# Optimization experiments

Hardware: AMD Instinct MI355X
Metric: run time of the kernel (lower is better)

Reference implementation:

```python
import jax, jax.numpy as jnp
import numpy as np

COMMITMENT_COST = 0.25
NUM_EMBEDDINGS = 1024
EMBEDDING_DIM = 64


def setup_inputs() -> dict:
    key = jax.random.key(0)
    k1, k2 = jax.random.split(key)
    x = jax.random.normal(k1, (32, 64, 64, 64), dtype=jnp.float32)
    embeddings = jax.random.normal(k2, (EMBEDDING_DIM, NUM_EMBEDDINGS), dtype=jnp.float32)
    return {"x": x, "embeddings": embeddings}


def reference(x, embeddings):
    # x: [..., D], embeddings: [D, K]
    flat = jnp.reshape(x, (-1, EMBEDDING_DIM))                       # [N, D]
    # squared euclidean distances via ||a||^2 - 2 a.e + ||e||^2      # [N, K]
    distances = (jnp.sum(flat * flat, axis=1, keepdims=True)
                 - 2.0 * (flat @ embeddings)
                 + jnp.sum(embeddings * embeddings, axis=0, keepdims=True))
    flat_indices = jnp.argmax(-distances, axis=1)                    # [N]
    encodings = jax.nn.one_hot(flat_indices, NUM_EMBEDDINGS, dtype=distances.dtype)  # [N, K]
    encoding_indices = jnp.reshape(flat_indices, x.shape[:-1])
    # gather codebook rows: embeddings.T[idx]
    quantized = jnp.take(embeddings.T, encoding_indices, axis=0)     # same shape as x
    e_latent_loss = jnp.mean((jax.lax.stop_gradient(quantized) - x) ** 2)
    q_latent_loss = jnp.mean((quantized - jax.lax.stop_gradient(x)) ** 2)
    loss = q_latent_loss + COMMITMENT_COST * e_latent_loss
    quantized_st = x + jax.lax.stop_gradient(quantized - x)          # straight-through
    avg_probs = jnp.mean(encodings, axis=0)                          # [K]
    perplexity = jnp.exp(-jnp.sum(avg_probs * jnp.log(avg_probs + 1e-10)))
    return quantized_st, loss, perplexity, encodings, encoding_indices, distances
```

## Files before the change

### kernel.cpp

```cpp
#include <hip/hip_runtime.h>
#include <hip/hip_bf16.h>
#include <math.h>

#define NROWS 131072
#define DDIM  64
#define KCODE 1024
#define TAU_B 0.008f

#define OFF_Q    0L
#define OFF_LOSS 8388608L
#define OFF_PERP 8388609L
#define OFF_ENC  8388610L
#define OFF_IDX  (OFF_ENC + 134217728L)
#define OFF_DIST (OFF_IDX + 131072L)

#define WS_ENORM 0L
#define WS_ET    1024L
#define WS_EBPH  66560L
#define WS_EBPL  99328L
#define WS_IDX   132096L
#define WS_CNT   263168L
#define WS_PART  395268L

typedef short bf16x8 __attribute__((ext_vector_type(8)));
typedef float f32x4  __attribute__((ext_vector_type(4)));
typedef float f32x2  __attribute__((ext_vector_type(2)));
typedef _Float16 f16x4v __attribute__((ext_vector_type(4)));

__device__ inline unsigned short f2bf(float f) {
    unsigned u = __float_as_uint(f);
    unsigned r = (u + 0x7fffu + ((u >> 16) & 1u)) >> 16;
    return (unsigned short)r;
}
__device__ inline float bf2f(unsigned short h) {
    return __uint_as_float(((unsigned)h) << 16);
}
__device__ inline int dswz16(int i) { return i ^ (((i >> 12) & 3) << 3); }

__global__ __launch_bounds__(256) void k1a_prep(const float* __restrict__ e,
                                                float* __restrict__ enorm,
                                                float* __restrict__ eT,
                                                int* __restrict__ cnt) {
    int k = blockIdx.x * 256 + threadIdx.x;
    float s = 0.f;
    #pragma unroll 8
    for (int d = 0; d < DDIM; ++d) {
        float v = e[(size_t)d * KCODE + k];
        s = fmaf(v, v, s);
        eT[(size_t)k * DDIM + d] = v;
    }
    enorm[k] = s;
    cnt[k] = 0;
}

__global__ __launch_bounds__(128) void k1b_pack(const float* __restrict__ e,
                                                unsigned short* __restrict__ ebph,
                                                unsigned short* __restrict__ ebpl) {
    const int gct = blockIdx.x;
    const int ks  = threadIdx.x >> 6;
    const int l   = threadIdx.x & 63;
    const int col = (gct << 4) | (l & 15);
    const int kb  = (ks << 5) + ((l >> 4) << 3);
    const size_t ob = ((size_t)((gct << 1) | ks) * 64 + l) * 8;
    #pragma unroll
    for (int j = 0; j < 8; ++j) {
        float f = e[(size_t)(kb + j) * KCODE + col];
        unsigned short h = f2bf(f);
        float lo = f - bf2f(h);
        ebph[ob + j] = h;
        ebpl[ob + j] = f2bf(lo);
    }
}

__global__ __launch_bounds__(256, 4) void kA_dist(const float* __restrict__ x,
                                                  const float* __restrict__ e,
                                                  const unsigned short* __restrict__ ebph,
                                                  const unsigned short* __restrict__ ebpl,
                                                  const float* __restrict__ enorm,
                                                  float* __restrict__ dist,
                                                  int* __restrict__ idxarr,
                                                  int* __restrict__ cnt,
                                                  float* __restrict__ partials) {
    __shared__ __align__(16) _Float16 dtH[16384];
    __shared__ float hd[2];
    __shared__ short xh[16 * 64];
    __shared__ short xl[16 * 64];
    __shared__ float xn[16];
    __shared__ float wm1[4][16], wm2[4][16];
    __shared__ int   wi1[4][16];
    __shared__ float ps[16];
    __shared__ int   sidx[16];
    __shared__ int   nearmask;
    __shared__ float xsh[DDIM];
    __shared__ double wbv[4];
    __shared__ int    wbi[4];

    const int tid  = threadIdx.x;
    const int lane = tid & 63;
    const int w    = tid >> 6;
    const int rowbase = blockIdx.x * 16;

    {
        if (tid == 0) nearmask = 0;
        float4 v = ((const float4*)(x + (size_t)rowbase * DDIM))[tid];
        int fi = tid * 4, r = fi >> 6, c = fi & 63;
        float fv[4] = {v.x, v.y, v.z, v.w};
        short hv[4], lv[4];
        #pragma unroll
        for (int q = 0; q < 4; ++q) {
            unsigned short hh = f2bf(fv[q]);
            hv[q] = (short)hh;
            lv[q] = (short)f2bf(fv[q] - bf2f(hh));
        }
        *(short4*)&xh[r * 64 + c] = make_short4(hv[0], hv[1], hv[2], hv[3]);
        *(short4*)&xl[r * 64 + c] = make_short4(lv[0], lv[1], lv[2], lv[3]);
        float s4 = fmaf(v.x, v.x, fmaf(v.y, v.y, fmaf(v.z, v.z, v.w * v.w)));
        #pragma unroll
        for (int m = 1; m < 16; m <<= 1) s4 += __shfl_xor(s4, m);
        if ((lane & 15) == 0) xn[r] = s4;
    }
    __syncthreads();

    const int arow = lane & 15, akb = (lane >> 4) << 3;
    bf16x8 ah0 = *(const bf16x8*)&xh[arow * 64 + akb];
    bf16x8 ah1 = *(const bf16x8*)&xh[arow * 64 + 32 + akb];
    bf16x8 al0 = *(const bf16x8*)&xl[arow * 64 + akb];
    bf16x8 al1 = *(const bf16x8*)&xl[arow * 64 + 32 + akb];

    const int wr   = (lane >> 4) << 2;
    const int colb = (w << 8) | (lane & 15);
    float xnv[4];
    #pragma unroll
    for (int r = 0; r < 4; ++r) xnv[r] = xn[wr + r];
    float env[16];
    #pragma unroll
    for (int ct = 0; ct < 16; ++ct) env[ct] = enorm[colb + (ct << 4)];

    float m1[4], m2[4];
    int   i1[4];
    #pragma unroll
    for (int r = 0; r < 4; ++r) { m1[r] = 3.4e38f; m2[r] = 3.4e38f; i1[r] = 1 << 30; }

    #pragma unroll 4
    for (int ct = 0; ct < 16; ++ct) {
        const int gct = (w << 4) | ct;
        const size_t bo = ((size_t)(gct << 1) * 64 + lane) * 8;
        bf16x8 bh0 = *(const bf16x8*)(ebph + bo);
        bf16x8 bh1 = *(const bf16x8*)(ebph + bo + 512);
        bf16x8 bl0 = *(const bf16x8*)(ebpl + bo);
        bf16x8 bl1 = *(const bf16x8*)(ebpl + bo + 512);

        f32x4 d = {0.f, 0.f, 0.f, 0.f};
        d = __builtin_amdgcn_mfma_f32_16x16x32_bf16(ah0, bh0, d, 0, 0, 0);
        d = __builtin_amdgcn_mfma_f32_16x16x32_bf16(ah1, bh1, d, 0, 0, 0);
        d = __builtin_amdgcn_mfma_f32_16x16x32_bf16(ah0, bl0, d, 0, 0, 0);
        d = __builtin_amdgcn_mfma_f32_16x16x32_bf16(ah1, bl1, d, 0, 0, 0);
        d = __builtin_amdgcn_mfma_f32_16x16x32_bf16(al0, bh0, d, 0, 0, 0);
        d = __builtin_amdgcn_mfma_f32_16x16x32_bf16(al1, bh1, d, 0, 0, 0);

        const int col = colb + (ct << 4);
        #pragma unroll
        for (int r = 0; r < 4; ++r) {
            float o = fmaf(-2.f, d[r], xnv[r] + env[ct]);
            if (o < m1[r]) { m2[r] = m1[r]; m1[r] = o; i1[r] = col; }
            else if (o < m2[r]) m2[r] = o;
            const int fl = ((wr + r) << 10) + col;
            if (fl >= 2) dtH[dswz16(fl - 2)] = (_Float16)o;
            else         hd[fl] = o;
        }
    }

    #pragma unroll
    for (int m = 1; m < 16; m <<= 1) {
        #pragma unroll
        for (int r = 0; r < 4; ++r) {
            float om1 = __shfl_xor(m1[r], m);
            int   oi1 = __shfl_xor(i1[r], m);
            float om2 = __shfl_xor(m2[r], m);
            if (om1 < m1[r] || (om1 == m1[r] && oi1 < i1[r])) {
                m2[r] = fminf(m1[r], om2); m1[r] = om1; i1[r] = oi1;
            } else {
                m2[r] = fminf(m2[r], om1);
            }
        }
    }
    if ((lane & 15) == 0) {
        #pragma unroll
        for (int r = 0; r < 4; ++r) {
            wm1[w][wr + r] = m1[r];
            wm2[w][wr + r] = m2[r];
            wi1[w][wr + r] = i1[r];
        }
    }
    __syncthreads();
    if (tid < 16) {
        float bm1 = wm1[0][tid], bm2 = wm2[0][tid];
        int   bi  = wi1[0][tid];
        #pragma unroll
        for (int wv = 1; wv < 4; ++wv) {
            float om1 = wm1[wv][tid], om2 = wm2[wv][tid];
            int   oi  = wi1[wv][tid];
            if (om1 < bm1 || (om1 == bm1 && oi < bi)) {
                bm2 = fminf(bm1, om2); bm1 = om1; bi = oi;
            } else {
                bm2 = fminf(bm2, om1);
            }
        }
        sidx[tid] = bi;
        ps[tid]   = bm1;
        if (bm2 - bm1 < TAU_B) atomicOr(&nearmask, 1 << tid);
    }
    __syncthreads();

    {
        float* dbase = dist + ((size_t)rowbase << 10);
        #pragma unroll
        for (int j = 0; j < 16; ++j) {
            const int s = (j << 8) + tid;
            if (s < 4095) {
                const int i0 = s << 2;
                const int iw = dswz16(i0);
                f16x4v h = *(const f16x4v*)&dtH[iw];
                f32x4 v = {(float)h[0], (float)h[1], (float)h[2], (float)h[3]};
                *(f32x4*)(dbase + 2 + i0) = v;
            }
        }
        if (tid == 255) {
            const int it = dswz16(16380);
            *(f32x2*)(dbase)         = (f32x2){hd[0], hd[1]};
            *(f32x2*)(dbase + 16382) = (f32x2){(float)dtH[it], (float)dtH[it + 1]};
        }
    }

    if (nearmask) {
        for (int mrow = nearmask; mrow; mrow &= (mrow - 1)) {
            const int r = __ffs(mrow) - 1;
            if (tid < DDIM) xsh[tid] = x[(size_t)(rowbase + r) * DDIM + tid];
            __syncthreads();
            const int k0 = tid * 4;
            double dd[4] = {0.0, 0.0, 0.0, 0.0};
            for (int d = 0; d < DDIM; ++d) {
                double xd = (double)xsh[d];
                float4 ev = *(const float4*)(e + (size_t)d * KCODE + k0);
                double t0 = xd - (double)ev.x; dd[0] = fma(t0, t0, dd[0]);
                double t1 = xd - (double)ev.y; dd[1] = fma(t1, t1, dd[1]);
                double t2 = xd - (double)ev.z; dd[2] = fma(t2, t2, dd[2]);
                double t3 = xd - (double)ev.w; dd[3] = fma(t3, t3, dd[3]);
            }
            double best = dd[0]; int bidx = k0;
            #pragma unroll
            for (int c = 1; c < 4; ++c)
                if (dd[c] < best) { best = dd[c]; bidx = k0 + c; }
            #pragma unroll
            for (int m = 1; m < 64; m <<= 1) {
                double ob = __shfl_xor(best, m);
                int    oi = __shfl_xor(bidx, m);
                if (ob < best || (ob == best && oi < bidx)) { best = ob; bidx = oi; }
            }
            if (lane == 0) { wbv[w] = best; wbi[w] = bidx; }
            __syncthreads();
            if (tid == 0) {
                double bb = wbv[0]; int bi = wbi[0];
                #pragma unroll
                for (int wv = 1; wv < 4; ++wv)
                    if (wbv[wv] < bb || (wbv[wv] == bb && wbi[wv] < bi)) {
                        bb = wbv[wv]; bi = wbi[wv];
                    }
                sidx[r] = bi; ps[r] = (float)bb;
            }
            __syncthreads();
        }
    }

    if (tid < 16) {
        const int idx = sidx[tid];
        idxarr[rowbase + tid] = idx;
        atomicAdd(cnt + idx, 1);
    }
    if (tid == 64) {
        float s = 0.f;
        #pragma unroll
        for (int j = 0; j < 16; ++j) s += ps[j];
        partials[blockIdx.x] = s;
    }
}

__global__ __launch_bounds__(256) void kC_final(const float* __restrict__ eT,
                                                const int* __restrict__ idxarr,
                                                float* __restrict__ outq,
                                                float* __restrict__ enc,
                                                float* __restrict__ outidx) {
    __shared__ int sidx[64];
    const int tid = threadIdx.x;
    const int rowbase = blockIdx.x * 64;

    if (tid < 64) {
        const int grow = rowbase + tid;
        const int idx = idxarr[grow];
        sidx[tid] = idx;
        outidx[grow] = (float)idx;
    }
    __syncthreads();

    #pragma unroll
    for (int it = 0; it < 4; ++it) {
        const int row = (it << 4) + (tid >> 4);
        const int grow = rowbase + row;
        const int idx = sidx[row];
        f32x4 ev = *(const f32x4*)(eT + (size_t)idx * DDIM + ((tid & 15) << 2));
        *((f32x4*)(outq + ((size_t)grow << 6)) + (tid & 15)) = ev;
    }

    float* ebase = enc + ((size_t)rowbase << 10);
    #pragma unroll 8
    for (int j = 0; j < 64; ++j) {
        const int s = (j << 8) + tid;
        if (s < 16383) {
            const int fb = 2 + (s << 2);
            const int r0 = fb >> 10, c0 = fb & 1023;
            const int i0 = sidx[r0];
            f32x4 v;
            if (c0 != 1022) {
                v.x = (c0     == i0) ? 1.f : 0.f;
                v.y = (c0 + 1 == i0) ? 1.f : 0.f;
                v.z = (c0 + 2 == i0) ? 1.f : 0.f;
                v.w = (c0 + 3 == i0) ? 1.f : 0.f;
            } else {
                const int i1b = sidx[r0 + 1];
                v.x = (1022 == i0)  ? 1.f : 0.f;
                v.y = (1023 == i0)  ? 1.f : 0.f;
                v.z = (0    == i1b) ? 1.f : 0.f;
                v.w = (1    == i1b) ? 1.f : 0.f;
            }
            *(f32x4*)(ebase + fb) = v;
        }
    }
    if (tid == 255) {
        f32x2 h, t;
        h.x = (0 == sidx[0]) ? 1.f : 0.f;
        h.y = (1 == sidx[0]) ? 1.f : 0.f;
        t.x = (1022 == sidx[63]) ? 1.f : 0.f;
        t.y = (1023 == sidx[63]) ? 1.f : 0.f;
        *(f32x2*)(ebase) = h;
        *(f32x2*)(ebase + 65534) = t;
    }
}

__global__ __launch_bounds__(256) void k6_scalar(const float* __restrict__ partials,
                                                 const int* __restrict__ cnt,
                                                 float* __restrict__ outloss,
                                                 float* __restrict__ outperp) {
    __shared__ double sd[256];
    const int tid = threadIdx.x;
    double s = 0.0;
    for (int i = tid; i < 8192; i += 256) s += (double)partials[i];
    sd[tid] = s;
    __syncthreads();
    for (int st = 128; st > 0; st >>= 1) {
        if (tid < st) sd[tid] += sd[tid + st];
        __syncthreads();
    }
    const double total = sd[0];
    __syncthreads();
    double h = 0.0;
    for (int k = tid; k < KCODE; k += 256) {
        double p = (double)cnt[k] / (double)NROWS;
        h -= p * log(p + 1e-10);
    }
    sd[tid] = h;
    __syncthreads();
    for (int st = 128; st > 0; st >>= 1) {
        if (tid < st) sd[tid] += sd[tid + st];
        __syncthreads();
    }
    if (tid == 0) {
        *outloss = (float)(total * 1.25 / (double)((long)NROWS * DDIM));
        *outperp = (float)exp(sd[0]);
    }
}

extern "C" void kernel_launch(void* const* d_in, const int* in_sizes, int n_in,
                              void* d_out, int out_size, void* d_ws, size_t ws_size,
                              hipStream_t stream) {
    const float* x = (const float*)d_in[0];
    const float* e = (const float*)d_in[1];
    float* out = (float*)d_out;

    float* ws_f = (float*)d_ws;
    float* enorm   = ws_f + WS_ENORM;
    float* eT      = ws_f + WS_ET;
    unsigned short* ebph = (unsigned short*)(ws_f + WS_EBPH);
    unsigned short* ebpl = (unsigned short*)(ws_f + WS_EBPL);
    int*   idxarr  = (int*)(ws_f + WS_IDX);
    int*   cnt     = (int*)(ws_f + WS_CNT);
    float* partials= ws_f + WS_PART;

    float* outq    = out + OFF_Q;
    float* outloss = out + OFF_LOSS;
    float* outperp = out + OFF_PERP;
    float* enc     = out + OFF_ENC;
    float* outidx  = out + OFF_IDX;
    float* dist    = out + OFF_DIST;

    hipLaunchKernelGGL(k1a_prep, dim3(4),    dim3(256), 0, stream, e, enorm, eT, cnt);
    hipLaunchKernelGGL(k1b_pack, dim3(64),   dim3(128), 0, stream, e, ebph, ebpl);
    hipLaunchKernelGGL(kA_dist,  dim3(8192), dim3(256), 0, stream, x, e, ebph, ebpl, enorm,
                       dist, idxarr, cnt, partials);
    hipLaunchKernelGGL(kC_final, dim3(2048), dim3(256), 0, stream, eT, idxarr, outq, enc, outidx);
    hipLaunchKernelGGL(k6_scalar,dim3(1),    dim3(256), 0, stream, partials, cnt, outloss, outperp);
}
```

Before: 339.9 us.

## Swap MFMA operands and write distances directly from registers, dropping LDS staging

Swaps the MFMA A/B operands so each lane holds four consecutive codebook columns for a single row. The fp32 distances can then go straight from registers to global memory as 8-byte stores, with no fp16 LDS staging buffer and no separate copy-out pass. Codebook norms are cached in LDS and read as float4, and the per-row min reduction becomes a cross-lane shuffle over the row groups. The aim is to cut LDS traffic, the fp16 truncation of stored distances and a block-wide pass, but the direct stores are narrower and strided across rows, which may lower write coalescing.

```diff
diff --git a/kernel.cpp b/kernel.cpp
--- a/kernel.cpp
+++ b/kernel.cpp
@@ -25,7 +25,6 @@
 typedef short bf16x8 __attribute__((ext_vector_type(8)));
 typedef float f32x4  __attribute__((ext_vector_type(4)));
 typedef float f32x2  __attribute__((ext_vector_type(2)));
-typedef _Float16 f16x4v __attribute__((ext_vector_type(4)));
 
 __device__ inline unsigned short f2bf(float f) {
     unsigned u = __float_as_uint(f);
@@ -35,7 +34,6 @@
 __device__ inline float bf2f(unsigned short h) {
     return __uint_as_float(((unsigned)h) << 16);
 }
-__device__ inline int dswz16(int i) { return i ^ (((i >> 12) & 3) << 3); }
 
 __global__ __launch_bounds__(256) void k1a_prep(const float* __restrict__ e,
                                                 float* __restrict__ enorm,
@@ -81,10 +79,9 @@
                                                   int* __restrict__ idxarr,
                                                   int* __restrict__ cnt,
                                                   float* __restrict__ partials) {
-    __shared__ __align__(16) _Float16 dtH[16384];
-    __shared__ float hd[2];
     __shared__ short xh[16 * 64];
     __shared__ short xl[16 * 64];
+    __shared__ float enl[KCODE];
     __shared__ float xn[16];
     __shared__ float wm1[4][16], wm2[4][16];
     __shared__ int   wi1[4][16];
@@ -118,6 +115,7 @@
         #pragma unroll
         for (int m = 1; m < 16; m <<= 1) s4 += __shfl_xor(s4, m);
         if ((lane & 15) == 0) xn[r] = s4;
+        ((float4*)enl)[tid] = ((const float4*)enorm)[tid];
     }
     __syncthreads();
 
@@ -127,19 +125,13 @@
     bf16x8 al0 = *(const bf16x8*)&xl[arow * 64 + akb];
     bf16x8 al1 = *(const bf16x8*)&xl[arow * 64 + 32 + akb];
 
-    const int wr   = (lane >> 4) << 2;
-    const int colb = (w << 8) | (lane & 15);
-    float xnv[4];
-    #pragma unroll
-    for (int r = 0; r < 4; ++r) xnv[r] = xn[wr + r];
-    float env[16];
-    #pragma unroll
-    for (int ct = 0; ct < 16; ++ct) env[ct] = enorm[colb + (ct << 4)];
-
-    float m1[4], m2[4];
-    int   i1[4];
-    #pragma unroll
-    for (int r = 0; r < 4; ++r) { m1[r] = 3.4e38f; m2[r] = 3.4e38f; i1[r] = 1 << 30; }
+    const int xr = lane & 15;
+    const int wr = (lane >> 4) << 2;
+    const float xnv = xn[xr];
+    float* drow = dist + (size_t)(rowbase + xr) * KCODE + (w << 8) + wr;
+
+    float m1 = 3.4e38f, m2 = 3.4e38f;
+    int   i1 = 1 << 30;
 
     #pragma unroll 4
     for (int ct = 0; ct < 16; ++ct) {
@@ -151,47 +143,41 @@
         bf16x8 bl1 = *(const bf16x8*)(ebpl + bo + 512);
 
         f32x4 d = {0.f, 0.f, 0.f, 0.f};
-        d = __builtin_amdgcn_mfma_f32_16x16x32_bf16(ah0, bh0, d, 0, 0, 0);
-        d = __builtin_amdgcn_mfma_f32_16x16x32_bf16(ah1, bh1, d, 0, 0, 0);
-        d = __builtin_amdgcn_mfma_f32_16x16x32_bf16(ah0, bl0, d, 0, 0, 0);
-        d = __builtin_amdgcn_mfma_f32_16x16x32_bf16(ah1, bl1, d, 0, 0, 0);
-        d = __builtin_amdgcn_mfma_f32_16x16x32_bf16(al0, bh0, d, 0, 0, 0);
-        d = __builtin_amdgcn_mfma_f32_16x16x32_bf16(al1, bh1, d, 0, 0, 0);
-
-        const int col = colb + (ct << 4);
-        #pragma unroll
-        for (int r = 0; r < 4; ++r) {
-            float o = fmaf(-2.f, d[r], xnv[r] + env[ct]);
-            if (o < m1[r]) { m2[r] = m1[r]; m1[r] = o; i1[r] = col; }
-            else if (o < m2[r]) m2[r] = o;
-            const int fl = ((wr + r) << 10) + col;
-            if (fl >= 2) dtH[dswz16(fl - 2)] = (_Float16)o;
-            else         hd[fl] = o;
-        }
+        d = __builtin_amdgcn_mfma_f32_16x16x32_bf16(bh0, ah0, d, 0, 0, 0);
+        d = __builtin_amdgcn_mfma_f32_16x16x32_bf16(bh1, ah1, d, 0, 0, 0);
+        d = __builtin_amdgcn_mfma_f32_16x16x32_bf16(bl0, ah0, d, 0, 0, 0);
+        d = __builtin_amdgcn_mfma_f32_16x16x32_bf16(bl1, ah1, d, 0, 0, 0);
+        d = __builtin_amdgcn_mfma_f32_16x16x32_bf16(bh0, al0, d, 0, 0, 0);
+        d = __builtin_amdgcn_mfma_f32_16x16x32_bf16(bh1, al1, d, 0, 0, 0);
+
+        const int cb = (w << 8) + (ct << 4) + wr;
+        f32x4 en4 = *(const f32x4*)&enl[cb];
+        float o0 = fmaf(-2.f, d[0], xnv + en4[0]);
+        float o1 = fmaf(-2.f, d[1], xnv + en4[1]);
+        float o2 = fmaf(-2.f, d[2], xnv + en4[2]);
+        float o3 = fmaf(-2.f, d[3], xnv + en4[3]);
+
+        *(f32x2*)(drow + (ct << 4))     = (f32x2){o0, o1};
+        *(f32x2*)(drow + (ct << 4) + 2) = (f32x2){o2, o3};
+
+        if (o0 < m1) { m2 = m1; m1 = o0; i1 = cb; }     else if (o0 < m2) m2 = o0;
+        if (o1 < m1) { m2 = m1; m1 = o1; i1 = cb + 1; } else if (o1 < m2) m2 = o1;
+        if (o2 < m1) { m2 = m1; m1 = o2; i1 = cb + 2; } else if (o2 < m2) m2 = o2;
+        if (o3 < m1) { m2 = m1; m1 = o3; i1 = cb + 3; } else if (o3 < m2) m2 = o3;
     }
 
     #pragma unroll
-    for (int m = 1; m < 16; m <<= 1) {
-        #pragma unroll
-        for (int r = 0; r < 4; ++r) {
-            float om1 = __shfl_xor(m1[r], m);
-            int   oi1 = __shfl_xor(i1[r], m);
-            float om2 = __shfl_xor(m2[r], m);
-            if (om1 < m1[r] || (om1 == m1[r] && oi1 < i1[r])) {
-                m2[r] = fminf(m1[r], om2); m1[r] = om1; i1[r] = oi1;
-            } else {
-                m2[r] = fminf(m2[r], om1);
-            }
-        }
-    }
-    if ((lane & 15) == 0) {
-        #pragma unroll
-        for (int r = 0; r < 4; ++r) {
-            wm1[w][wr + r] = m1[r];
-            wm2[w][wr + r] = m2[r];
-            wi1[w][wr + r] = i1[r];
-        }
-    }
+    for (int m = 16; m < 64; m <<= 1) {
+        float om1 = __shfl_xor(m1, m);
+        int   oi1 = __shfl_xor(i1, m);
+        float om2 = __shfl_xor(m2, m);
+        if (om1 < m1 || (om1 == m1 && oi1 < i1)) {
+            m2 = fminf(m1, om2); m1 = om1; i1 = oi1;
+        } else {
+            m2 = fminf(m2, om1);
+        }
+    }
+    if (lane < 16) { wm1[w][lane] = m1; wm2[w][lane] = m2; wi1[w][lane] = i1; }
     __syncthreads();
     if (tid < 16) {
         float bm1 = wm1[0][tid], bm2 = wm2[0][tid];
@@ -211,26 +197,6 @@
         if (bm2 - bm1 < TAU_B) atomicOr(&nearmask, 1 << tid);
     }
     __syncthreads();
-
-    {
-        float* dbase = dist + ((size_t)rowbase << 10);
-        #pragma unroll
-        for (int j = 0; j < 16; ++j) {
-            const int s = (j << 8) + tid;
-            if (s < 4095) {
-                const int i0 = s << 2;
-                const int iw = dswz16(i0);
-                f16x4v h = *(const f16x4v*)&dtH[iw];
-                f32x4 v = {(float)h[0], (float)h[1], (float)h[2], (float)h[3]};
-                *(f32x4*)(dbase + 2 + i0) = v;
-            }
-        }
-        if (tid == 255) {
-            const int it = dswz16(16380);
-            *(f32x2*)(dbase)         = (f32x2){hd[0], hd[1]};
-            *(f32x2*)(dbase + 16382) = (f32x2){(float)dtH[it], (float)dtH[it + 1]};
-        }
-    }
 
     if (nearmask) {
         for (int mrow = nearmask; mrow; mrow &= (mrow - 1)) {
```

Measured after the change: 406.0 us. +19.4%, slower.
